# Optimization experiments

Measured on AMD Instinct MI355X. Metric: run time of the kernel, lower is better.

The kernel has to match this reference:

```python
import jax, jax.numpy as jnp
import numpy as np

NUM_NODES = 50000
NUM_EDGES = 640000
H_DIM = 128
OUT_DIM = 128
NUM_RELS = 16
NUM_BASES = 8


def _rgcn_layer(h, basis, coef, bias, src, dst, etype, norm, activation):
    # Basis decomposition: W[r] = sum_b coef[r,b] * basis[b]  -> [R, d_in, d_out]
    W = jnp.einsum('rb,bio->rio', coef, basis)
    # Transform node features under every relation: [R, N, d_out]
    Hr = jnp.einsum('ni,rio->rno', h, W)
    # Per-edge message: pick (relation, source) pair, apply edge norm. [E, d_out]
    msg = Hr[etype, src] * norm
    # Aggregate messages at destination nodes. [N, d_out]
    out = jax.ops.segment_sum(msg, dst, num_segments=h.shape[0])
    out = out + bias
    return activation(out) if activation is not None else out


def setup_inputs() -> dict:
    key = jax.random.key(0)
    ks = jax.random.split(key, 10)
    h = jax.random.normal(ks[0], (NUM_NODES, H_DIM), dtype=jnp.float32)
    norm = jax.random.uniform(ks[1], (NUM_EDGES, 1), dtype=jnp.float32)
    src = jax.random.randint(ks[2], (NUM_EDGES,), 0, NUM_NODES, dtype=jnp.int32)
    dst = jax.random.randint(ks[3], (NUM_EDGES,), 0, NUM_NODES, dtype=jnp.int32)
    etype = jax.random.randint(ks[4], (NUM_EDGES,), 0, NUM_RELS, dtype=jnp.int32)
    s1 = 1.0 / np.sqrt(H_DIM)
    s2 = 1.0 / np.sqrt(H_DIM)
    V1 = jax.random.normal(ks[5], (NUM_BASES, H_DIM, H_DIM), dtype=jnp.float32) * s1
    coef1 = jax.random.normal(ks[6], (NUM_RELS, NUM_BASES), dtype=jnp.float32) * (1.0 / np.sqrt(NUM_BASES))
    bias1 = jnp.zeros((H_DIM,), dtype=jnp.float32)
    V2 = jax.random.normal(ks[7], (NUM_BASES, H_DIM, OUT_DIM), dtype=jnp.float32) * s2
    coef2 = jax.random.normal(ks[8], (NUM_RELS, NUM_BASES), dtype=jnp.float32) * (1.0 / np.sqrt(NUM_BASES))
    bias2 = jnp.zeros((OUT_DIM,), dtype=jnp.float32)
    return {
        'h': h, 'norm': norm, 'src': src, 'dst': dst, 'etype': etype,
        'V1': V1, 'coef1': coef1, 'bias1': bias1,
        'V2': V2, 'coef2': coef2, 'bias2': bias2,
    }


def reference(h, norm, src, dst, etype, V1, coef1, bias1, V2, coef2, bias2):
    # Layer 0: relational graph conv with ReLU (hidden layer)
    h1 = _rgcn_layer(h, V1, coef1, bias1, src, dst, etype, norm, jax.nn.relu)
    # Layer 1+: BaseRGCN sorts edges by relation (bucketing for the low-mem
    # per-relation dispatch). The sort is a permutation of the edge set, so we
    # mirror it explicitly; the segment_sum result is mathematically identical.
    order = jnp.argsort(etype)
    src_s, dst_s, et_s, norm_s = src[order], dst[order], etype[order], norm[order]
    out = _rgcn_layer(h1, V2, coef2, bias2, src_s, dst_s, et_s, norm_s, None)
    return out
```

## Files before the change

### kernel.cpp

```cpp
#include <hip/hip_runtime.h>

#define N_RELS 16
#define N_BASES 8
#define HD 128
#define SCAN_B 1024
#define ROWS 32

typedef __attribute__((ext_vector_type(8))) short bf16x8;
typedef __attribute__((ext_vector_type(4))) float floatx4;

__device__ __forceinline__ short bf16rn(float f) {
    union { float f; unsigned u; } v; v.f = f;
    unsigned u = v.u;
    unsigned r = (u + 0x7fffu + ((u >> 16) & 1u)) >> 16;
    return (short)r;
}


__global__ void hist_dst(const int* __restrict__ dst, int E, int* __restrict__ cnt) {
    int i = blockIdx.x * blockDim.x + threadIdx.x;
    if (i < E) atomicAdd(&cnt[dst[i]], 1);
}

__global__ void scan_partial(const int* __restrict__ cnt, int N,
                             int* __restrict__ excl, int* __restrict__ bsum) {
    __shared__ int s[SCAN_B];
    int t = threadIdx.x, i = blockIdx.x * SCAN_B + t;
    int v = (i < N) ? cnt[i] : 0;
    s[t] = v; __syncthreads();
    for (int o = 1; o < SCAN_B; o <<= 1) {
        int x = (t >= o) ? s[t - o] : 0;
        __syncthreads();
        s[t] += x;
        __syncthreads();
    }
    if (i < N) excl[i] = s[t] - v;
    if (t == SCAN_B - 1) bsum[blockIdx.x] = s[t];
}

__global__ void scan_bsum(int* __restrict__ bsum, int nb, int* __restrict__ row_ptr,
                          int N, int E) {
    if (threadIdx.x == 0 && blockIdx.x == 0) {
        int run = 0;
        for (int b = 0; b < nb; b++) { int x = bsum[b]; bsum[b] = run; run += x; }
        row_ptr[N] = E;
    }
}

__global__ void scan_fixup(int* __restrict__ row_ptr, const int* __restrict__ bsum,
                           int N, int* __restrict__ cursor) {
    int i = blockIdx.x * blockDim.x + threadIdx.x;
    if (i < N) { int v = row_ptr[i] + bsum[i >> 10]; row_ptr[i] = v; cursor[i] = v; }
}

__global__ void scatter_dst(const int* __restrict__ dst, const int* __restrict__ src,
                            const int* __restrict__ et, const float* __restrict__ norm,
                            int E, int* __restrict__ cursor, int2* __restrict__ edata) {
    int i = blockIdx.x * blockDim.x + threadIdx.x;
    if (i >= E) return;
    int p = atomicAdd(&cursor[dst[i]], 1);
    edata[p] = make_int2((et[i] << 16) | src[i], __float_as_int(norm[i]));
}


__global__ void pack_bf16(const float* __restrict__ x, unsigned* __restrict__ o, int n2) {
    int i = blockIdx.x * blockDim.x + threadIdx.x;
    if (i >= n2) return;
    float2 v = ((const float2*)x)[i];
    o[i] = ((unsigned)(unsigned short)bf16rn(v.y) << 16) | (unsigned short)bf16rn(v.x);
}


__global__ void compute_V_frags(const float* __restrict__ V1, const float* __restrict__ V2,
                                short* __restrict__ Vf) {
    int blk = blockIdx.x;
    const float* V = ((blk & 8) ? V2 : V1) + (size_t)(blk & 7) * 16384;
    size_t obase = (size_t)blk * 16384;
    for (int e = threadIdx.x; e < 16384; e += blockDim.x) {
        float w = V[e];
        int k = e >> 7, n = e & 127;
        int kk = k >> 5, q = (k >> 3) & 3, j = k & 7;
        int lane = q * 16 + (n & 15);
        int idx = ((kk * 8 + (n >> 4)) * 64 + lane) * 8 + j;
        Vf[obase + idx] = bf16rn(w);
    }
}


__global__ __launch_bounds__(512, 4) void rgcn_tile(
    const unsigned* __restrict__ hb, const int2* __restrict__ edata,
    const int* __restrict__ row_ptr, const float* __restrict__ coef,
    const short* __restrict__ Vf, const float* __restrict__ bias,
    void* __restrict__ outp, int N, int mode) {
    __shared__ __align__(16) unsigned Zs[N_BASES][4][4][ROWS + 1][4];

    const int tid = threadIdx.x;
    const int wave = tid >> 6, lane = tid & 63;
    const int nb0 = blockIdx.x * ROWS;

    const int lkk = lane >> 4, lq = (lane >> 2) & 3, lju = lane & 3;

    for (int i = 0; i < 4; i++) {
        const int row = wave * 4 + i;
        const int node = nb0 + row;
        int e = 0, end = 0;
        if (node < N) { e = row_ptr[node]; end = row_ptr[node + 1]; }

        float2 acc[N_BASES] = {};
        auto proc = [&](int2 m, unsigned g) {
            int ets = __builtin_amdgcn_readfirstlane(m.x >> 16);
            float nv = __int_as_float(m.y);
            const float* cw = coef + ets * N_BASES;
            float vx = __uint_as_float(g << 16) * nv;
            float vy = __uint_as_float(g & 0xffff0000u) * nv;
#pragma unroll
            for (int b = 0; b < N_BASES; b++) {
                float w = cw[b];
                acc[b].x = fmaf(vx, w, acc[b].x);
                acc[b].y = fmaf(vy, w, acc[b].y);
            }
        };

        for (; e + 4 <= end; e += 4) {
            int2 m0 = edata[e], m1 = edata[e + 1], m2 = edata[e + 2], m3 = edata[e + 3];
            unsigned g0 = hb[(size_t)(m0.x & 0xffff) * 64 + lane];
            unsigned g1 = hb[(size_t)(m1.x & 0xffff) * 64 + lane];
            unsigned g2 = hb[(size_t)(m2.x & 0xffff) * 64 + lane];
            unsigned g3 = hb[(size_t)(m3.x & 0xffff) * 64 + lane];
            proc(m0, g0); proc(m1, g1); proc(m2, g2); proc(m3, g3);
        }
        for (; e < end; e++) {
            int2 m = edata[e];
            unsigned g = hb[(size_t)(m.x & 0xffff) * 64 + lane];
            proc(m, g);
        }

#pragma unroll
        for (int b = 0; b < N_BASES; b++) {
            unsigned lo = (unsigned)(unsigned short)bf16rn(acc[b].x);
            unsigned hi = (unsigned)(unsigned short)bf16rn(acc[b].y);
            Zs[b][lkk][lq][row][lju] = (hi << 16) | lo;
        }
    }
    __syncthreads();

    const int q = lane >> 4, cc = lane & 15;
    const int tt = wave;
    floatx4 ac0 = {}, ac1 = {};

#pragma unroll 2
    for (int b = 0; b < N_BASES; b++) {
#pragma unroll
        for (int kk = 0; kk < 4; kk++) {
            bf16x8 a0 = *(const bf16x8*)&Zs[b][kk][q][cc][0];
            bf16x8 a1 = *(const bf16x8*)&Zs[b][kk][q][16 + cc][0];
            bf16x8 B = *(const bf16x8*)(Vf + (size_t)b * 16384 +
                                        ((size_t)(kk * 8 + tt) * 64 + lane) * 8);
            ac0 = __builtin_amdgcn_mfma_f32_16x16x32_bf16(a0, B, ac0, 0, 0, 0);
            ac1 = __builtin_amdgcn_mfma_f32_16x16x32_bf16(a1, B, ac1, 0, 0, 0);
        }
    }

    float bv = bias[tt * 16 + cc];
    if (mode == 0) {
        unsigned short* o = (unsigned short*)outp;
#pragma unroll
        for (int mi = 0; mi < 2; mi++) {
            const floatx4& c = mi ? ac1 : ac0;
#pragma unroll
            for (int i = 0; i < 4; i++) {
                int node = nb0 + mi * 16 + q * 4 + i;
                if (node < N) {
                    float v = fmaxf(c[i] + bv, 0.f);
                    o[(size_t)node * HD + tt * 16 + cc] = (unsigned short)bf16rn(v);
                }
            }
        }
    } else {
        float* o = (float*)outp;
#pragma unroll
        for (int mi = 0; mi < 2; mi++) {
            const floatx4& c = mi ? ac1 : ac0;
#pragma unroll
            for (int i = 0; i < 4; i++) {
                int node = nb0 + mi * 16 + q * 4 + i;
                if (node < N) o[(size_t)node * HD + tt * 16 + cc] = c[i] + bv;
            }
        }
    }
}


extern "C" void kernel_launch(void* const* d_in, const int* in_sizes, int n_in,
                              void* d_out, int out_size, void* d_ws, size_t ws_size,
                              hipStream_t stream) {
    const float* h     = (const float*)d_in[0];
    const float* norm  = (const float*)d_in[1];
    const int*   src   = (const int*)d_in[2];
    const int*   dst   = (const int*)d_in[3];
    const int*   etype = (const int*)d_in[4];
    const float* V1    = (const float*)d_in[5];
    const float* coef1 = (const float*)d_in[6];
    const float* bias1 = (const float*)d_in[7];
    const float* V2    = (const float*)d_in[8];
    const float* coef2 = (const float*)d_in[9];
    const float* bias2 = (const float*)d_in[10];
    const int N = in_sizes[0] / HD;
    const int E = in_sizes[2];
    float* out = (float*)d_out;
    (void)n_in; (void)out_size; (void)ws_size;

    char* ws = (char*)d_ws;
    size_t off = 0;
    auto alloc = [&](size_t bytes) {
        void* p = ws + off;
        off += (bytes + 255) & ~(size_t)255;
        return p;
    };
    short*    Vf      = (short*)alloc((size_t)16 * 16384 * sizeof(short));
    unsigned* hb      = (unsigned*)alloc((size_t)N * 64 * sizeof(unsigned));
    unsigned* h1b     = (unsigned*)alloc((size_t)N * 64 * sizeof(unsigned));
    int2*     edata   = (int2*)alloc((size_t)E * sizeof(int2));
    int*      cnt     = (int*)alloc((size_t)N * sizeof(int));
    int*      row_ptr = (int*)alloc((size_t)(N + 1) * sizeof(int));
    int*      cursor  = (int*)alloc((size_t)N * sizeof(int));
    int*      bsum    = (int*)alloc(256 * sizeof(int));

    const int nb = (N + SCAN_B - 1) / SCAN_B;

    hipMemsetAsync(cnt, 0, (size_t)N * sizeof(int), stream);
    hist_dst<<<(E + 255) / 256, 256, 0, stream>>>(dst, E, cnt);
    scan_partial<<<nb, SCAN_B, 0, stream>>>(cnt, N, row_ptr, bsum);
    scan_bsum<<<1, 64, 0, stream>>>(bsum, nb, row_ptr, N, E);
    scan_fixup<<<(N + 255) / 256, 256, 0, stream>>>(row_ptr, bsum, N, cursor);
    scatter_dst<<<(E + 255) / 256, 256, 0, stream>>>(dst, src, etype, norm, E, cursor, edata);
    compute_V_frags<<<16, 256, 0, stream>>>(V1, V2, Vf);
    pack_bf16<<<(N * 64 + 255) / 256, 256, 0, stream>>>(h, hb, N * 64);

    const int tiles = (N + ROWS - 1) / ROWS;

    rgcn_tile<<<tiles, 512, 0, stream>>>(hb, edata, row_ptr, coef1, Vf, bias1, h1b, N, 0);
    rgcn_tile<<<tiles, 512, 0, stream>>>(h1b, edata, row_ptr, coef2, Vf + (size_t)8 * 16384,
                                         bias2, out, N, 1);
}
```

Measured before the change: 363.3 us.

## Fuse setup kernels, fold block-sum scan into fixup, balance rows dynamically

Merges bf16 packing, V fragment construction and the dst histogram into one launch, and folds the serial block-sum scan into the fixup kernel through a wave shuffle scan. Within each tile, waves now take rows from a shared atomic ticket instead of a fixed four rows each, which balances uneven node degrees. The per-basis accumulation is rewritten with 2-wide float vectors so the compiler can emit packed FMAs. These cut launch count and wave imbalance, at the cost of an LDS atomic per row and the fixup scan assuming at most 64 scan blocks.

```diff
diff --git a/kernel.cpp b/kernel.cpp
--- a/kernel.cpp
+++ b/kernel.cpp
@@ -8,6 +8,7 @@
 
 typedef __attribute__((ext_vector_type(8))) short bf16x8;
 typedef __attribute__((ext_vector_type(4))) float floatx4;
+typedef __attribute__((ext_vector_type(2))) float floatx2;
 
 __device__ __forceinline__ short bf16rn(float f) {
     union { float f; unsigned u; } v; v.f = f;
@@ -17,10 +18,39 @@
 }
 
 
-__global__ void hist_dst(const int* __restrict__ dst, int E, int* __restrict__ cnt) {
-    int i = blockIdx.x * blockDim.x + threadIdx.x;
+__global__ void setup_fused(const float* __restrict__ h, unsigned* __restrict__ hb, int n2,
+                            const float* __restrict__ V1, const float* __restrict__ V2,
+                            short* __restrict__ Vf,
+                            const int* __restrict__ dst, int E, int* __restrict__ cnt,
+                            int packBlocks, int vBlocks) {
+    int blk = blockIdx.x;
+    if (blk < packBlocks) {
+        int i = blk * blockDim.x + threadIdx.x;
+        if (i < n2) {
+            float2 v = ((const float2*)h)[i];
+            hb[i] = ((unsigned)(unsigned short)bf16rn(v.y) << 16) | (unsigned short)bf16rn(v.x);
+        }
+        return;
+    }
+    blk -= packBlocks;
+    if (blk < vBlocks) {
+        const float* V = ((blk & 8) ? V2 : V1) + (size_t)(blk & 7) * 16384;
+        size_t obase = (size_t)blk * 16384;
+        for (int e = threadIdx.x; e < 16384; e += blockDim.x) {
+            float w = V[e];
+            int k = e >> 7, n = e & 127;
+            int kk = k >> 5, q = (k >> 3) & 3, j = k & 7;
+            int lane = q * 16 + (n & 15);
+            int idx = ((kk * 8 + (n >> 4)) * 64 + lane) * 8 + j;
+            Vf[obase + idx] = bf16rn(w);
+        }
+        return;
+    }
+    blk -= vBlocks;
+    int i = blk * blockDim.x + threadIdx.x;
     if (i < E) atomicAdd(&cnt[dst[i]], 1);
 }
+
 
 __global__ void scan_partial(const int* __restrict__ cnt, int N,
                              int* __restrict__ excl, int* __restrict__ bsum) {
@@ -38,19 +68,24 @@
     if (t == SCAN_B - 1) bsum[blockIdx.x] = s[t];
 }
 
-__global__ void scan_bsum(int* __restrict__ bsum, int nb, int* __restrict__ row_ptr,
-                          int N, int E) {
-    if (threadIdx.x == 0 && blockIdx.x == 0) {
-        int run = 0;
-        for (int b = 0; b < nb; b++) { int x = bsum[b]; bsum[b] = run; run += x; }
-        row_ptr[N] = E;
-    }
-}
-
 __global__ void scan_fixup(int* __restrict__ row_ptr, const int* __restrict__ bsum,
-                           int N, int* __restrict__ cursor) {
-    int i = blockIdx.x * blockDim.x + threadIdx.x;
-    if (i < N) { int v = row_ptr[i] + bsum[i >> 10]; row_ptr[i] = v; cursor[i] = v; }
+                           int nb, int N, int E, int* __restrict__ cursor) {
+    __shared__ int pref[64];
+    int t = threadIdx.x;
+    if (t < 64) {
+        int raw = (t < nb) ? bsum[t] : 0;
+        int v = raw;
+#pragma unroll
+        for (int o = 1; o < 64; o <<= 1) {
+            int u = __shfl_up(v, o, 64);
+            if (t >= o) v += u;
+        }
+        pref[t] = v - raw;
+    }
+    __syncthreads();
+    int i = blockIdx.x * blockDim.x + t;
+    if (i < N) { int val = row_ptr[i] + pref[i >> 10]; row_ptr[i] = val; cursor[i] = val; }
+    if (i == 0) row_ptr[N] = E;
 }
 
 __global__ void scatter_dst(const int* __restrict__ dst, const int* __restrict__ src,
@@ -63,62 +98,43 @@
 }
 
 
-__global__ void pack_bf16(const float* __restrict__ x, unsigned* __restrict__ o, int n2) {
-    int i = blockIdx.x * blockDim.x + threadIdx.x;
-    if (i >= n2) return;
-    float2 v = ((const float2*)x)[i];
-    o[i] = ((unsigned)(unsigned short)bf16rn(v.y) << 16) | (unsigned short)bf16rn(v.x);
-}
-
-
-__global__ void compute_V_frags(const float* __restrict__ V1, const float* __restrict__ V2,
-                                short* __restrict__ Vf) {
-    int blk = blockIdx.x;
-    const float* V = ((blk & 8) ? V2 : V1) + (size_t)(blk & 7) * 16384;
-    size_t obase = (size_t)blk * 16384;
-    for (int e = threadIdx.x; e < 16384; e += blockDim.x) {
-        float w = V[e];
-        int k = e >> 7, n = e & 127;
-        int kk = k >> 5, q = (k >> 3) & 3, j = k & 7;
-        int lane = q * 16 + (n & 15);
-        int idx = ((kk * 8 + (n >> 4)) * 64 + lane) * 8 + j;
-        Vf[obase + idx] = bf16rn(w);
-    }
-}
-
-
 __global__ __launch_bounds__(512, 4) void rgcn_tile(
     const unsigned* __restrict__ hb, const int2* __restrict__ edata,
     const int* __restrict__ row_ptr, const float* __restrict__ coef,
     const short* __restrict__ Vf, const float* __restrict__ bias,
     void* __restrict__ outp, int N, int mode) {
     __shared__ __align__(16) unsigned Zs[N_BASES][4][4][ROWS + 1][4];
+    __shared__ int ticket;
 
     const int tid = threadIdx.x;
     const int wave = tid >> 6, lane = tid & 63;
     const int nb0 = blockIdx.x * ROWS;
 
+    if (tid == 0) ticket = 0;
+    __syncthreads();
+
     const int lkk = lane >> 4, lq = (lane >> 2) & 3, lju = lane & 3;
 
-    for (int i = 0; i < 4; i++) {
-        const int row = wave * 4 + i;
+    for (;;) {
+        int row0 = 0;
+        if (lane == 0) row0 = atomicAdd(&ticket, 1);
+        const int row = __builtin_amdgcn_readfirstlane(row0);
+        if (row >= ROWS) break;
         const int node = nb0 + row;
         int e = 0, end = 0;
         if (node < N) { e = row_ptr[node]; end = row_ptr[node + 1]; }
 
-        float2 acc[N_BASES] = {};
+        floatx2 acc[N_BASES] = {};
         auto proc = [&](int2 m, unsigned g) {
             int ets = __builtin_amdgcn_readfirstlane(m.x >> 16);
             float nv = __int_as_float(m.y);
             const float* cw = coef + ets * N_BASES;
-            float vx = __uint_as_float(g << 16) * nv;
-            float vy = __uint_as_float(g & 0xffff0000u) * nv;
-#pragma unroll
-            for (int b = 0; b < N_BASES; b++) {
-                float w = cw[b];
-                acc[b].x = fmaf(vx, w, acc[b].x);
-                acc[b].y = fmaf(vy, w, acc[b].y);
-            }
+            floatx2 v;
+            v.x = __uint_as_float(g << 16) * nv;
+            v.y = __uint_as_float(g & 0xffff0000u) * nv;
+#pragma unroll
+            for (int b = 0; b < N_BASES; b++)
+                acc[b] = v * cw[b] + acc[b];
         };
 
         for (; e + 4 <= end; e += 4) {
@@ -227,15 +243,16 @@
     int*      bsum    = (int*)alloc(256 * sizeof(int));
 
     const int nb = (N + SCAN_B - 1) / SCAN_B;
+    const int packBlocks = (N * 64 + 255) / 256;
+    const int vBlocks = 16;
+    const int histBlocks = (E + 255) / 256;
 
     hipMemsetAsync(cnt, 0, (size_t)N * sizeof(int), stream);
-    hist_dst<<<(E + 255) / 256, 256, 0, stream>>>(dst, E, cnt);
+    setup_fused<<<packBlocks + vBlocks + histBlocks, 256, 0, stream>>>(
+        h, hb, N * 64, V1, V2, Vf, dst, E, cnt, packBlocks, vBlocks);
     scan_partial<<<nb, SCAN_B, 0, stream>>>(cnt, N, row_ptr, bsum);
-    scan_bsum<<<1, 64, 0, stream>>>(bsum, nb, row_ptr, N, E);
-    scan_fixup<<<(N + 255) / 256, 256, 0, stream>>>(row_ptr, bsum, N, cursor);
+    scan_fixup<<<(N + 255) / 256, 256, 0, stream>>>(row_ptr, bsum, nb, N, E, cursor);
     scatter_dst<<<(E + 255) / 256, 256, 0, stream>>>(dst, src, etype, norm, E, cursor, edata);
-    compute_V_frags<<<16, 256, 0, stream>>>(V1, V2, Vf);
-    pack_bf16<<<(N * 64 + 255) / 256, 256, 0, stream>>>(h, hb, N * 64);
 
     const int tiles = (N + ROWS - 1) / ROWS;
 
```

After: 320.5 us. -11.8%, faster.
